# Kernel optimization log

Hardware: AMD Instinct MI355X
Metric: run time of the kernel (lower is better)

Reference implementation:

```python
import jax, jax.numpy as jnp
import numpy as np

B, S, D = 4, 2048, 1024
H = 16
HD = D // H
PF = 4096
EPS = 1e-5


def setup_inputs() -> dict:
    key = jax.random.key(0)
    ks = jax.random.split(key, 16)
    s = 1.0 / np.sqrt(D)
    inp = {
        'src': jax.random.normal(ks[0], (B, S, D), jnp.float32),
        'Wq': jax.random.normal(ks[1], (D, D), jnp.float32) * s,
        'bq': jnp.zeros((D,), jnp.float32),
        'Wk': jax.random.normal(ks[2], (D, D), jnp.float32) * s,
        'bk': jnp.zeros((D,), jnp.float32),
        'Wv': jax.random.normal(ks[3], (D, D), jnp.float32) * s,
        'bv': jnp.zeros((D,), jnp.float32),
        'Wo': jax.random.normal(ks[4], (D, D), jnp.float32) * s,
        'bo': jnp.zeros((D,), jnp.float32),
        'g1': jnp.ones((D,), jnp.float32),
        'b1': jnp.zeros((D,), jnp.float32),
        'W1': jax.random.normal(ks[5], (D, PF), jnp.float32) * s,
        'bf1': jnp.zeros((PF,), jnp.float32),
        'W2': jax.random.normal(ks[6], (PF, D), jnp.float32) * (1.0 / np.sqrt(PF)),
        'bf2': jnp.zeros((D,), jnp.float32),
        'g2': jnp.ones((D,), jnp.float32),
        'b2': jnp.zeros((D,), jnp.float32),
    }
    return inp


def _layer_norm(x, g, b):
    mu = jnp.mean(x, axis=-1, keepdims=True)
    var = jnp.mean(jnp.square(x - mu), axis=-1, keepdims=True)
    return (x - mu) * jax.lax.rsqrt(var + EPS) * g + b


def reference(src, Wq, bq, Wk, bk, Wv, bv, Wo, bo, g1, b1, W1, bf1, W2, bf2, g2, b2):
    scale = 1.0 / np.sqrt(HD)
    # QKV projections -> [B, H, S, HD]
    q = (src @ Wq + bq).reshape(B, S, H, HD).transpose(0, 2, 1, 3)
    k = (src @ Wk + bk).reshape(B, S, H, HD).transpose(0, 2, 1, 3)
    v = (src @ Wv + bv).reshape(B, S, H, HD).transpose(0, 2, 1, 3)
    # attention scores [B, H, S, S]
    attn = jax.nn.softmax(jnp.einsum('bhqd,bhkd->bhqk', q, k) * scale, axis=-1)
    x = jnp.einsum('bhqk,bhkd->bhqd', attn, v)
    x = x.transpose(0, 2, 1, 3).reshape(B, S, D)
    attn_out = x @ Wo + bo
    # residual + LN (dropout is identity at p=0)
    src1 = _layer_norm(src + attn_out, g1, b1)
    # positionwise FFN: Linear -> Dropout -> ReLU -> Linear
    ff = jax.nn.relu(src1 @ W1 + bf1) @ W2 + bf2
    return _layer_norm(src1 + ff, g2, b2)
```

## Files before the change

kernel.cpp:

```cpp
#include <hip/hip_runtime.h>

#define BB 4
#define SS 2048
#define DD 1024
#define HH 16
#define PFF 4096
#define MR 8192

typedef unsigned short u16;
typedef __attribute__((ext_vector_type(8))) short s16x8;
typedef __attribute__((ext_vector_type(4))) float f32x4v;
typedef __attribute__((ext_vector_type(16))) float f32x16;
typedef __attribute__((ext_vector_type(4))) unsigned short u16x4;
typedef __attribute__((ext_vector_type(8))) unsigned short u16x8;

__device__ inline u16 f2bf(float f) {
  union { float f; unsigned u; } v; v.f = f;
  unsigned r = v.u + 0x7FFFu + ((v.u >> 16) & 1u);
  return (u16)(r >> 16);
}

__device__ inline unsigned cvtpk_bf16(float lo, float hi) {
  unsigned r;
  asm("v_cvt_pk_bf16_f32 %0, %1, %2" : "=v"(r) : "v"(lo), "v"(hi));
  return r;
}

__device__ inline void gload16(const void* g, void* l) {
  __builtin_amdgcn_global_load_lds(
      (const __attribute__((address_space(1))) void*)g,
      (__attribute__((address_space(3))) void*)l, 16, 0, 0);
}

__device__ inline f32x4v MFMA(s16x8 a, s16x8 b, f32x4v c) {
  return __builtin_amdgcn_mfma_f32_16x16x32_bf16(a, b, c, 0, 0, 0);
}
__device__ inline f32x16 MFMA32(s16x8 a, s16x8 b, f32x16 c) {
  return __builtin_amdgcn_mfma_f32_32x32x16_bf16(a, b, c, 0, 0, 0);
}

#define RAWBAR()                          \
  do {                                    \
    asm volatile("" ::: "memory");        \
    __builtin_amdgcn_s_barrier();         \
    asm volatile("" ::: "memory");        \
  } while (0)
#define WAITVM(N) asm volatile("s_waitcnt vmcnt(" #N ")" ::: "memory")

__device__ inline s16x8 ldfrag(const u16* base, int row, int colByte) {
  return *(const s16x8*)((const char*)base + row * 128 + (colByte ^ ((row & 7) << 4)));
}

template <int BN, int RELU, int OUTBF, int SCQ>
__global__ __launch_bounds__(512, 1) void gemm256(
    const u16* __restrict__ A, const u16* __restrict__ Bt,
    const float* __restrict__ bias, float* __restrict__ Cf,
    u16* __restrict__ Cb, int M, int N, int K, int ntx) {
  constexpr int WM = (BN == 256) ? 8 : 4;
  constexpr int HM = WM / 2;
  constexpr int BUF = 8192 + BN * 32;
  __shared__ __align__(128) u16 lds[3 * BUF];
  const int t = threadIdx.x;
  const int lane = t & 63, w = t >> 6;
  const int wr = (BN == 256) ? (w >> 2) : (w >> 1);
  const int wc = (BN == 256) ? (w & 3) : (w & 1);
  const int g = lane >> 4, q = lane & 15;

  const int cpx = gridDim.x >> 3;
  const int wg = (blockIdx.x & 7) * cpx + (blockIdx.x >> 3);
  const int row0 = (wg / ntx) * 256, col0 = (wg % ntx) * BN;

  f32x4v acc[WM][4];
#pragma unroll
  for (int m = 0; m < WM; ++m)
#pragma unroll
    for (int n = 0; n < 4; ++n) acc[m][n] = (f32x4v){0.f, 0.f, 0.f, 0.f};

  const int sr0 = t >> 2, sc0 = (t & 3) * 8;
  const u16* Ag0 = A + (size_t)(row0 + sr0) * K + sc0;
  const u16* Ag1 = A + (size_t)(row0 + sr0 + 128) * K + sc0;
  const u16* Bg0 = Bt + (size_t)(col0 + sr0) * K + sc0;
  const u16* Bg1 = Bt + (size_t)(col0 + sr0 + 128) * K + sc0;
  const int wud = (t & ~63) * 8;

#define STAGE_A(kt, buf)                                          \
  do {                                                            \
    u16* ab_ = &lds[(buf) * BUF];                                 \
    gload16(Ag0 + (kt) * 32, ab_ + wud);                          \
    gload16(Ag1 + (kt) * 32, ab_ + 4096 + wud);                   \
  } while (0)
#define STAGE_B(kt, buf)                                          \
  do {                                                            \
    u16* bb_ = &lds[(buf) * BUF + 8192];                          \
    gload16(Bg0 + (kt) * 32, bb_ + wud);                          \
    if (BN == 256) gload16(Bg1 + (kt) * 32, bb_ + 4096 + wud);    \
  } while (0)

  const int NT = K / 32;
  STAGE_A(0, 0); STAGE_B(0, 0);
  STAGE_A(1, 1); STAGE_B(1, 1);
  if constexpr (BN == 256) WAITVM(4); else WAITVM(3);
  RAWBAR();

  int cur = 0, nxt = 2;
  for (int kt = 0; kt < NT; ++kt) {
    const u16* ab = &lds[cur * BUF];
    const u16* bb = ab + 8192;
    const bool pf = (kt + 2 < NT);
    if (pf) STAGE_A(kt + 2, nxt);
    s16x8 bf_[4], af_[HM];
#pragma unroll
    for (int n = 0; n < 4; ++n)
      bf_[n] = *(const s16x8*)&bb[(wc * 64 + n * 16 + q) * 32 + g * 8];
#pragma unroll
    for (int m = 0; m < HM; ++m)
      af_[m] = *(const s16x8*)&ab[(wr * (WM * 16) + m * 16 + q) * 32 + g * 8];
    RAWBAR();
    __builtin_amdgcn_s_setprio(1);
#pragma unroll
    for (int m = 0; m < HM; ++m)
#pragma unroll
      for (int n = 0; n < 4; ++n) acc[m][n] = MFMA(af_[m], bf_[n], acc[m][n]);
    __builtin_amdgcn_s_setprio(0);
    RAWBAR();
    if (pf) STAGE_B(kt + 2, nxt);
#pragma unroll
    for (int m = 0; m < HM; ++m)
      af_[m] = *(const s16x8*)&ab[(wr * (WM * 16) + (m + HM) * 16 + q) * 32 + g * 8];
    RAWBAR();
    __builtin_amdgcn_s_setprio(1);
#pragma unroll
    for (int m = 0; m < HM; ++m)
#pragma unroll
      for (int n = 0; n < 4; ++n)
        acc[m + HM][n] = MFMA(af_[m], bf_[n], acc[m + HM][n]);
    __builtin_amdgcn_s_setprio(0);
    if (kt + 1 < NT) {
      if (pf) {
        if constexpr (BN == 256) WAITVM(4); else WAITVM(3);
      } else {
        WAITVM(0);
      }
    }
    RAWBAR();
    cur = (cur == 2) ? 0 : cur + 1;
    nxt = (nxt == 2) ? 0 : nxt + 1;
  }
#undef STAGE_A
#undef STAGE_B

#pragma unroll
  for (int n = 0; n < 4; ++n) {
    const int col = col0 + wc * 64 + 16 * n + q;
    const float bv = bias[col];
#pragma unroll
    for (int m = 0; m < WM; ++m) {
#pragma unroll
      for (int r = 0; r < 4; ++r) {
        const int row = row0 + wr * (WM * 16) + 16 * m + 4 * g + r;
        float v = acc[m][n][r] + bv;
        if (RELU) v = fmaxf(v, 0.f);
        if (SCQ && col < DD) v *= 0.18033688011112042f;
        if (OUTBF) Cb[(size_t)row * N + col] = f2bf(v);
        else Cf[(size_t)row * N + col] = v;
      }
    }
  }
}

__global__ __launch_bounds__(256, 4) void attn_mfma(
    const u16* __restrict__ qkv, const u16* __restrict__ vt,
    u16* __restrict__ xb) {
  __shared__ __align__(128) u16 lds[16384];

  const int t = threadIdx.x;
  const int w = t >> 6, lane = t & 63;
  const int q = lane & 31, hi = lane >> 5;
  const int qg = w >> 1;
  const int kg = w & 1;

  const int flat = blockIdx.x;
  const int xcd = flat & 7;
  const int j = flat >> 3;
  const int bh = xcd * 8 + (j & 7);
  const int qb = j >> 3;
  const int b = bh >> 4, h = bh & 15;
  const int q0 = qb * 64;
  const int qcol = h * 64, kcol = DD + h * 64;

  const int r0 = t >> 3;
  const int sc = ((t & 7) ^ (r0 & 7)) * 8;
  const int ldst = (t & ~63) * 16;
  const u16* Ksrc = qkv + (size_t)(b * SS + r0) * 3072 + kcol + sc;
  const u16* Vsrc = vt + (size_t)(bh * 64 + r0) * SS + sc;

  {
    const u16* Qsrc = qkv + (size_t)(b * SS + q0 + r0) * 3072 + qcol + sc;
    gload16(Qsrc, (char*)lds + ldst);
    gload16(Qsrc + (size_t)32 * 3072, (char*)lds + 4096 + ldst);
  }
  WAITVM(0);
  RAWBAR();
  s16x8 qf[4];
  {
    const u16* Qw = lds + qg * 2048;
#pragma unroll
    for (int s = 0; s < 4; ++s) qf[s] = ldfrag(Qw, q, 32 * s + 16 * hi);
  }
  asm volatile("s_waitcnt lgkmcnt(0)" ::: "memory");
  __builtin_amdgcn_sched_barrier(0);
  RAWBAR();

  gload16(Ksrc, (char*)lds + ldst);
  gload16(Ksrc + (size_t)32 * 3072, (char*)lds + 4096 + ldst);
  gload16(Vsrc, (char*)lds + 8192 + ldst);
  gload16(Vsrc + 32 * SS, (char*)lds + 12288 + ldst);
  WAITVM(0);
  RAWBAR();

  s16x8 onesv;
#pragma unroll
  for (int i = 0; i < 8; ++i) onesv[i] = (short)0x3F80;

  f32x16 zf;
#pragma unroll
  for (int i = 0; i < 16; ++i) zf[i] = 0.f;

  f32x16 oac0, oac1, lacc;
#pragma unroll
  for (int i = 0; i < 16; ++i) { oac0[i] = 0.f; oac1[i] = 0.f; lacc[i] = 0.f; }

  for (int kt = 0; kt < SS / 64; ++kt) {
    const int cur = kt & 1;
    const u16* Kc = lds + cur * 8192;
    const u16* Vc = Kc + 4096;
    if (kt + 1 < SS / 64) {
      const size_t ko = (size_t)(kt + 1) * 64 * 3072;
      const int vo = (kt + 1) * 64;
      char* base = (char*)lds + (cur ^ 1) * 16384;
      gload16(Ksrc + ko, base + ldst);
      gload16(Ksrc + ko + (size_t)32 * 3072, base + 4096 + ldst);
      gload16(Vsrc + vo, base + 8192 + ldst);
      gload16(Vsrc + vo + 32 * SS, base + 12288 + ldst);
    }

    __builtin_amdgcn_s_setprio(1);
    s16x8 k0 = ldfrag(Kc, kg * 32 + q, 16 * hi);
    f32x16 sa = MFMA32(k0, qf[0], zf);
#pragma unroll
    for (int s = 1; s < 4; ++s) {
      s16x8 ks = ldfrag(Kc, kg * 32 + q, 32 * s + 16 * hi);
      sa = MFMA32(ks, qf[s], sa);
    }
    __builtin_amdgcn_s_setprio(0);

#pragma unroll
    for (int i = 0; i < 16; ++i) sa[i] = exp2f(sa[i]);

    __builtin_amdgcn_s_setprio(1);
#pragma unroll
    for (int sp = 0; sp < 2; ++sp) {
      const int rb = 8 * sp;
      unsigned x0 = cvtpk_bf16(sa[rb + 0], sa[rb + 1]);
      unsigned x1 = cvtpk_bf16(sa[rb + 2], sa[rb + 3]);
      unsigned y0 = cvtpk_bf16(sa[rb + 4], sa[rb + 5]);
      unsigned y1 = cvtpk_bf16(sa[rb + 6], sa[rb + 7]);
      asm("v_permlane32_swap_b32 %0, %1" : "+v"(x0), "+v"(y0));
      asm("v_permlane32_swap_b32 %0, %1" : "+v"(x1), "+v"(y1));
      union { unsigned u[4]; s16x8 v; } pf;
      pf.u[0] = x0; pf.u[1] = x1; pf.u[2] = y0; pf.u[3] = y1;
      s16x8 v0 = ldfrag(Vc, q, kg * 64 + 32 * sp + 16 * hi);
      s16x8 v1 = ldfrag(Vc, 32 + q, kg * 64 + 32 * sp + 16 * hi);
      oac0 = MFMA32(v0, pf.v, oac0);
      oac1 = MFMA32(v1, pf.v, oac1);
      lacc = MFMA32(onesv, pf.v, lacc);
    }
    __builtin_amdgcn_s_setprio(0);

    WAITVM(0);
    RAWBAR();
  }

  __syncthreads();
  float* red = (float*)lds;
  if (kg == 1) {
    float* myr = red + (qg * 64 + lane) * 33;
#pragma unroll
    for (int i = 0; i < 16; ++i) { myr[i] = oac0[i]; myr[16 + i] = oac1[i]; }
    myr[32] = lacc[0];
  }
  __syncthreads();
  if (kg == 0) {
    const float* pr = red + (qg * 64 + lane) * 33;
#pragma unroll
    for (int i = 0; i < 16; ++i) { oac0[i] += pr[i]; oac1[i] += pr[16 + i]; }
    const float inv = 1.f / (lacc[0] + pr[32]);
    const size_t row = (size_t)(b * SS + q0 + qg * 32 + q);
    u16* orow = xb + row * DD + qcol;
#pragma unroll
    for (int rr = 0; rr < 4; ++rr) {
      uint2 pw0, pw1;
      pw0.x = cvtpk_bf16(oac0[4 * rr] * inv, oac0[4 * rr + 1] * inv);
      pw0.y = cvtpk_bf16(oac0[4 * rr + 2] * inv, oac0[4 * rr + 3] * inv);
      pw1.x = cvtpk_bf16(oac1[4 * rr] * inv, oac1[4 * rr + 1] * inv);
      pw1.y = cvtpk_bf16(oac1[4 * rr + 2] * inv, oac1[4 * rr + 3] * inv);
      *(uint2*)(orow + 8 * rr + 4 * hi) = pw0;
      *(uint2*)(orow + 32 + 8 * rr + 4 * hi) = pw1;
    }
  }
}

__global__ __launch_bounds__(256) void cvt_bf16(const float* __restrict__ x,
                                                u16* __restrict__ y, int n4) {
  int i = blockIdx.x * 256 + threadIdx.x;
  if (i < n4) {
    float4 v = ((const float4*)x)[i];
    u16x4 o;
    o[0] = f2bf(v.x); o[1] = f2bf(v.y); o[2] = f2bf(v.z); o[3] = f2bf(v.w);
    ((u16x4*)y)[i] = o;
  }
}

__global__ __launch_bounds__(256) void transpose_w(const float* __restrict__ W,
                                                   u16* __restrict__ Wt,
                                                   int K, int N) {
  __shared__ float T[32][33];
  const int n0 = blockIdx.x * 32, k0 = blockIdx.y * 32;
  const int t = threadIdx.x;
  const int r = t >> 3, c = (t & 7) * 4;
  float4 v = *(const float4*)&W[(size_t)(k0 + r) * N + n0 + c];
  T[r][c] = v.x; T[r][c + 1] = v.y; T[r][c + 2] = v.z; T[r][c + 3] = v.w;
  __syncthreads();
  const int a = t >> 3, b0 = (t & 7) * 4;
  u16x4 o;
#pragma unroll
  for (int j = 0; j < 4; ++j) o[j] = f2bf(T[b0 + j][a]);
  *(u16x4*)&Wt[(size_t)(n0 + a) * K + k0 + b0] = o;
}

__global__ __launch_bounds__(256) void vtrans(const u16* __restrict__ qkv,
                                              u16* __restrict__ vt) {
  __shared__ u16 T[64 * 72];
  const int t = threadIdx.x;
  const int bh = blockIdx.y, b = bh >> 4, h = bh & 15;
  const int s0 = blockIdx.x * 64;
  const int vcol = 2048 + h * 64;
#pragma unroll
  for (int i = 0; i < 2; ++i) {
    int c = i * 256 + t;
    int sr = c >> 3, dc = (c & 7) * 8;
    *(u16x8*)&T[sr * 72 + dc] =
        *(const u16x8*)&qkv[(size_t)(b * SS + s0 + sr) * 3072 + vcol + dc];
  }
  __syncthreads();
#pragma unroll
  for (int i = 0; i < 2; ++i) {
    int c = i * 256 + t;
    int d = c >> 3, scnk = (c & 7) * 8;
    u16x8 o;
#pragma unroll
    for (int jj = 0; jj < 8; ++jj) o[jj] = T[(scnk + jj) * 72 + d];
    *(u16x8*)&vt[(size_t)(bh * 64 + d) * SS + s0 + scnk] = o;
  }
}

__global__ __launch_bounds__(256) void concat3(const float* __restrict__ a,
                                               const float* __restrict__ b,
                                               const float* __restrict__ c,
                                               float* __restrict__ o) {
  int i = blockIdx.x * 256 + threadIdx.x;
  if (i < 3072)
    o[i] = i < 1024 ? a[i] : (i < 2048 ? b[i - 1024] : c[i - 2048]);
}

template <int WB>
__global__ __launch_bounds__(256) void ln_res(
    const float* __restrict__ X, const float* __restrict__ R,
    const float* __restrict__ g, const float* __restrict__ b,
    float* __restrict__ Y, u16* __restrict__ Yb) {
  const int row = blockIdx.x;
  const int t = threadIdx.x;
  const size_t off = (size_t)row * DD + t * 4;

  float4 x4 = *(const float4*)&X[off];
  float4 r4 = *(const float4*)&R[off];
  float v0 = x4.x + r4.x, v1 = x4.y + r4.y, v2 = x4.z + r4.z, v3 = x4.w + r4.w;

  float s1 = v0 + v1 + v2 + v3;
  float s2 = v0 * v0 + v1 * v1 + v2 * v2 + v3 * v3;
#pragma unroll
  for (int o = 1; o < 64; o <<= 1) {
    s1 += __shfl_xor(s1, o);
    s2 += __shfl_xor(s2, o);
  }
  __shared__ float red1[4], red2[4];
  if ((t & 63) == 0) {
    red1[t >> 6] = s1;
    red2[t >> 6] = s2;
  }
  __syncthreads();
  s1 = red1[0] + red1[1] + red1[2] + red1[3];
  s2 = red2[0] + red2[1] + red2[2] + red2[3];

  const float mu = s1 * (1.f / DD);
  const float var = s2 * (1.f / DD) - mu * mu;
  const float rs = rsqrtf(var + 1e-5f);

  float4 g4 = *(const float4*)&g[t * 4];
  float4 b4 = *(const float4*)&b[t * 4];
  float4 y;
  y.x = (v0 - mu) * rs * g4.x + b4.x;
  y.y = (v1 - mu) * rs * g4.y + b4.y;
  y.z = (v2 - mu) * rs * g4.z + b4.z;
  y.w = (v3 - mu) * rs * g4.w + b4.w;
  *(float4*)&Y[off] = y;
  if (WB) {
    u16x4 o;
    o[0] = f2bf(y.x); o[1] = f2bf(y.y); o[2] = f2bf(y.z); o[3] = f2bf(y.w);
    *(u16x4*)&Yb[off] = o;
  }
}

extern "C" void kernel_launch(void* const* d_in, const int* in_sizes, int n_in,
                              void* d_out, int out_size, void* d_ws,
                              size_t ws_size, hipStream_t stream) {
  const float* src = (const float*)d_in[0];
  const float* Wq  = (const float*)d_in[1];
  const float* bq  = (const float*)d_in[2];
  const float* Wk  = (const float*)d_in[3];
  const float* bk  = (const float*)d_in[4];
  const float* Wv  = (const float*)d_in[5];
  const float* bv  = (const float*)d_in[6];
  const float* Wo  = (const float*)d_in[7];
  const float* bo  = (const float*)d_in[8];
  const float* g1  = (const float*)d_in[9];
  const float* b1  = (const float*)d_in[10];
  const float* W1  = (const float*)d_in[11];
  const float* bf1 = (const float*)d_in[12];
  const float* W2  = (const float*)d_in[13];
  const float* bf2 = (const float*)d_in[14];
  const float* g2  = (const float*)d_in[15];
  const float* b2  = (const float*)d_in[16];

  char* W = (char*)d_ws;
  u16*   wqkvT = (u16*)  (W + 0);
  u16*   woT   = (u16*)  (W + 6291456);
  u16*   w1T   = (u16*)  (W + 8388608);
  u16*   w2T   = (u16*)  (W + 16777216);
  float* bqkv  = (float*)(W + 25165824);
  u16*   srcb  = (u16*)  (W + 25178112);
  u16*   qkv   = (u16*)  (W + 41955328);
  u16*   vt    = (u16*)  (W + 92286976);
  u16*   xb    = (u16*)  (W + 109064192);
  float* pb    = (float*)(W + 125841408);
  float* s1f   = (float*)(W + 159395840);
  u16*   s1bb  = (u16*)  (W + 109064192);
  u16*   f1b   = (u16*)  (W + 41955328);
  float* f2b   = (float*)(W + 125841408);

  dim3 blk(256);

  cvt_bf16<<<8192, blk, 0, stream>>>(src, srcb, MR * DD / 4);
  transpose_w<<<dim3(32, 32), blk, 0, stream>>>(Wq, wqkvT, DD, DD);
  transpose_w<<<dim3(32, 32), blk, 0, stream>>>(Wk, wqkvT + (size_t)1024 * 1024, DD, DD);
  transpose_w<<<dim3(32, 32), blk, 0, stream>>>(Wv, wqkvT + (size_t)2048 * 1024, DD, DD);
  transpose_w<<<dim3(32, 32), blk, 0, stream>>>(Wo, woT, DD, DD);
  transpose_w<<<dim3(128, 32), blk, 0, stream>>>(W1, w1T, DD, PFF);
  transpose_w<<<dim3(32, 128), blk, 0, stream>>>(W2, w2T, PFF, DD);
  concat3<<<12, blk, 0, stream>>>(bq, bk, bv, bqkv);

  gemm256<256, 0, 1, 1><<<384, 512, 0, stream>>>(srcb, wqkvT, bqkv, nullptr,
                                                 qkv, MR, 3072, DD, 12);
  vtrans<<<dim3(32, 64), blk, 0, stream>>>(qkv, vt);
  attn_mfma<<<2048, 256, 0, stream>>>(qkv, vt, xb);
  gemm256<128, 0, 0, 0><<<256, 512, 0, stream>>>(xb, woT, bo, pb, nullptr,
                                                 MR, DD, DD, 8);
  ln_res<1><<<MR, blk, 0, stream>>>(src, pb, g1, b1, s1f, s1bb);
  gemm256<256, 1, 1, 0><<<512, 512, 0, stream>>>(s1bb, w1T, bf1, nullptr, f1b,
                                                 MR, PFF, DD, 16);
  gemm256<128, 0, 0, 0><<<256, 512, 0, stream>>>(f1b, w2T, bf2, f2b, nullptr,
                                                 MR, DD, PFF, 8);
  ln_res<0><<<MR, blk, 0, stream>>>(s1f, f2b, g2, b2, (float*)d_out, nullptr);
}
```

Measured before the change: 465.1 us.

## Triple-buffer K/V tiles in attention kernel with two-tile-deep prefetch

Moves the attention kernel's K/V staging from double to triple buffering in LDS, so loads run two tiles ahead and the end-of-iteration wait only covers the tile just consumed. This hides more global-load latency behind the MFMA work. In exchange LDS use per block rises from 32KB to 48KB and the occupancy hint drops from 4 to 3 blocks per CU, which could cut latency hiding across waves.

After: 465.6 us. About the same (+0.1%).

```diff
diff --git a/kernel.cpp b/kernel.cpp
--- a/kernel.cpp
+++ b/kernel.cpp
@@ -168,10 +168,10 @@
   }
 }
 
-__global__ __launch_bounds__(256, 4) void attn_mfma(
+__global__ __launch_bounds__(256, 3) void attn_mfma(
     const u16* __restrict__ qkv, const u16* __restrict__ vt,
     u16* __restrict__ xb) {
-  __shared__ __align__(128) u16 lds[16384];
+  __shared__ __align__(128) u16 lds[3 * 8192];
 
   const int t = threadIdx.x;
   const int w = t >> 6, lane = t & 63;
@@ -211,11 +211,20 @@
   __builtin_amdgcn_sched_barrier(0);
   RAWBAR();
 
-  gload16(Ksrc, (char*)lds + ldst);
-  gload16(Ksrc + (size_t)32 * 3072, (char*)lds + 4096 + ldst);
-  gload16(Vsrc, (char*)lds + 8192 + ldst);
-  gload16(Vsrc + 32 * SS, (char*)lds + 12288 + ldst);
-  WAITVM(0);
+#define STAGEKV(kt, bufidx)                                             \
+  do {                                                                  \
+    char* base_ = (char*)lds + (bufidx) * 16384;                        \
+    const size_t ko_ = (size_t)(kt) * 64 * 3072;                        \
+    const int vo_ = (kt) * 64;                                          \
+    gload16(Ksrc + ko_, base_ + ldst);                                  \
+    gload16(Ksrc + ko_ + (size_t)32 * 3072, base_ + 4096 + ldst);       \
+    gload16(Vsrc + vo_, base_ + 8192 + ldst);                           \
+    gload16(Vsrc + vo_ + 32 * SS, base_ + 12288 + ldst);                \
+  } while (0)
+
+  STAGEKV(0, 0);
+  STAGEKV(1, 1);
+  WAITVM(4);
   RAWBAR();
 
   s16x8 onesv;
@@ -230,19 +239,13 @@
 #pragma unroll
   for (int i = 0; i < 16; ++i) { oac0[i] = 0.f; oac1[i] = 0.f; lacc[i] = 0.f; }
 
-  for (int kt = 0; kt < SS / 64; ++kt) {
-    const int cur = kt & 1;
+  const int NT = SS / 64;
+  int cur = 0, nxt = 2;
+  for (int kt = 0; kt < NT; ++kt) {
+    const bool pf = (kt + 2 < NT);
+    if (pf) STAGEKV(kt + 2, nxt);
     const u16* Kc = lds + cur * 8192;
     const u16* Vc = Kc + 4096;
-    if (kt + 1 < SS / 64) {
-      const size_t ko = (size_t)(kt + 1) * 64 * 3072;
-      const int vo = (kt + 1) * 64;
-      char* base = (char*)lds + (cur ^ 1) * 16384;
-      gload16(Ksrc + ko, base + ldst);
-      gload16(Ksrc + ko + (size_t)32 * 3072, base + 4096 + ldst);
-      gload16(Vsrc + vo, base + 8192 + ldst);
-      gload16(Vsrc + vo + 32 * SS, base + 12288 + ldst);
-    }
 
     __builtin_amdgcn_s_setprio(1);
     s16x8 k0 = ldfrag(Kc, kg * 32 + q, 16 * hi);
@@ -267,19 +270,25 @@
       unsigned y1 = cvtpk_bf16(sa[rb + 6], sa[rb + 7]);
       asm("v_permlane32_swap_b32 %0, %1" : "+v"(x0), "+v"(y0));
       asm("v_permlane32_swap_b32 %0, %1" : "+v"(x1), "+v"(y1));
-      union { unsigned u[4]; s16x8 v; } pf;
-      pf.u[0] = x0; pf.u[1] = x1; pf.u[2] = y0; pf.u[3] = y1;
+      union { unsigned u[4]; s16x8 v; } pfv;
+      pfv.u[0] = x0; pfv.u[1] = x1; pfv.u[2] = y0; pfv.u[3] = y1;
       s16x8 v0 = ldfrag(Vc, q, kg * 64 + 32 * sp + 16 * hi);
       s16x8 v1 = ldfrag(Vc, 32 + q, kg * 64 + 32 * sp + 16 * hi);
-      oac0 = MFMA32(v0, pf.v, oac0);
-      oac1 = MFMA32(v1, pf.v, oac1);
-      lacc = MFMA32(onesv, pf.v, lacc);
+      oac0 = MFMA32(v0, pfv.v, oac0);
+      oac1 = MFMA32(v1, pfv.v, oac1);
+      lacc = MFMA32(onesv, pfv.v, lacc);
     }
     __builtin_amdgcn_s_setprio(0);
 
-    WAITVM(0);
+    if (kt + 1 < NT) {
+      if (pf) WAITVM(4);
+      else WAITVM(0);
+    }
     RAWBAR();
-  }
+    cur = (cur == 2) ? 0 : cur + 1;
+    nxt = (nxt == 2) ? 0 : nxt + 1;
+  }
+#undef STAGEKV
 
   __syncthreads();
   float* red = (float*)lds;
```

## Merge prep kernels and split-K the N=1024 GEMMs, folding partial sums into LayerNorm

Applied to the files above, without the earlier changes.

Merges the src conversion, the six weight transposes and the bias concat into one prep_all launch to cut launch overhead. When the workspace is large enough, the Wo and W2 GEMMs (N=1024, only 256 tiles) run as two sequential split-K halves writing separate fp32 partial outputs. The residual LayerNorm kernels then add the second partial. Each split GEMM has half the K loop, but the halves run back to back, so this adds launches and an extra fp32 partial write/read rather than more concurrency.

Result: slower. 480.9 us (+3.4%).

```diff
diff --git a/kernel.cpp b/kernel.cpp
--- a/kernel.cpp
+++ b/kernel.cpp
@@ -55,7 +55,7 @@
 __global__ __launch_bounds__(512, 1) void gemm256(
     const u16* __restrict__ A, const u16* __restrict__ Bt,
     const float* __restrict__ bias, float* __restrict__ Cf,
-    u16* __restrict__ Cb, int M, int N, int K, int ntx) {
+    u16* __restrict__ Cb, int M, int N, int K, int lda, int ntx) {
   constexpr int WM = (BN == 256) ? 8 : 4;
   constexpr int HM = WM / 2;
   constexpr int BUF = 8192 + BN * 32;
@@ -77,10 +77,10 @@
     for (int n = 0; n < 4; ++n) acc[m][n] = (f32x4v){0.f, 0.f, 0.f, 0.f};
 
   const int sr0 = t >> 2, sc0 = (t & 3) * 8;
-  const u16* Ag0 = A + (size_t)(row0 + sr0) * K + sc0;
-  const u16* Ag1 = A + (size_t)(row0 + sr0 + 128) * K + sc0;
-  const u16* Bg0 = Bt + (size_t)(col0 + sr0) * K + sc0;
-  const u16* Bg1 = Bt + (size_t)(col0 + sr0 + 128) * K + sc0;
+  const u16* Ag0 = A + (size_t)(row0 + sr0) * lda + sc0;
+  const u16* Ag1 = A + (size_t)(row0 + sr0 + 128) * lda + sc0;
+  const u16* Bg0 = Bt + (size_t)(col0 + sr0) * lda + sc0;
+  const u16* Bg1 = Bt + (size_t)(col0 + sr0 + 128) * lda + sc0;
   const int wud = (t & ~63) * 8;
 
 #define STAGE_A(kt, buf)                                          \
@@ -152,7 +152,7 @@
 #pragma unroll
   for (int n = 0; n < 4; ++n) {
     const int col = col0 + wc * 64 + 16 * n + q;
-    const float bv = bias[col];
+    const float bv = bias ? bias[col] : 0.f;
 #pragma unroll
     for (int m = 0; m < WM; ++m) {
 #pragma unroll
@@ -267,13 +267,13 @@
       unsigned y1 = cvtpk_bf16(sa[rb + 6], sa[rb + 7]);
       asm("v_permlane32_swap_b32 %0, %1" : "+v"(x0), "+v"(y0));
       asm("v_permlane32_swap_b32 %0, %1" : "+v"(x1), "+v"(y1));
-      union { unsigned u[4]; s16x8 v; } pf;
-      pf.u[0] = x0; pf.u[1] = x1; pf.u[2] = y0; pf.u[3] = y1;
+      union { unsigned u[4]; s16x8 v; } pfv;
+      pfv.u[0] = x0; pfv.u[1] = x1; pfv.u[2] = y0; pfv.u[3] = y1;
       s16x8 v0 = ldfrag(Vc, q, kg * 64 + 32 * sp + 16 * hi);
       s16x8 v1 = ldfrag(Vc, 32 + q, kg * 64 + 32 * sp + 16 * hi);
-      oac0 = MFMA32(v0, pf.v, oac0);
-      oac1 = MFMA32(v1, pf.v, oac1);
-      lacc = MFMA32(onesv, pf.v, lacc);
+      oac0 = MFMA32(v0, pfv.v, oac0);
+      oac1 = MFMA32(v1, pfv.v, oac1);
+      lacc = MFMA32(onesv, pfv.v, lacc);
     }
     __builtin_amdgcn_s_setprio(0);
 
@@ -310,23 +310,48 @@
   }
 }
 
-__global__ __launch_bounds__(256) void cvt_bf16(const float* __restrict__ x,
-                                                u16* __restrict__ y, int n4) {
-  int i = blockIdx.x * 256 + threadIdx.x;
-  if (i < n4) {
-    float4 v = ((const float4*)x)[i];
+__global__ __launch_bounds__(256) void prep_all(
+    const float* __restrict__ src, u16* __restrict__ srcb,
+    const float* __restrict__ Wq, const float* __restrict__ Wk,
+    const float* __restrict__ Wv, const float* __restrict__ Wo,
+    u16* __restrict__ wqkvT, u16* __restrict__ woT,
+    const float* __restrict__ W1, u16* __restrict__ w1T,
+    const float* __restrict__ W2, u16* __restrict__ w2T,
+    const float* __restrict__ bq, const float* __restrict__ bk,
+    const float* __restrict__ bvv, float* __restrict__ bqkv) {
+  const int id = blockIdx.x;
+  const int t = threadIdx.x;
+  __shared__ float T[32][33];
+
+  if (id < 8192) {
+    int i = id * 256 + t;
+    float4 v = ((const float4*)src)[i];
     u16x4 o;
     o[0] = f2bf(v.x); o[1] = f2bf(v.y); o[2] = f2bf(v.z); o[3] = f2bf(v.w);
-    ((u16x4*)y)[i] = o;
-  }
-}
-
-__global__ __launch_bounds__(256) void transpose_w(const float* __restrict__ W,
-                                                   u16* __restrict__ Wt,
-                                                   int K, int N) {
-  __shared__ float T[32][33];
-  const int n0 = blockIdx.x * 32, k0 = blockIdx.y * 32;
-  const int t = threadIdx.x;
+    ((u16x4*)srcb)[i] = o;
+    return;
+  }
+  const int id2 = id - 8192;
+  if (id2 >= 12288) {
+    int i = (id2 - 12288) * 256 + t;
+    if (i < 3072)
+      bqkv[i] = i < 1024 ? bq[i] : (i < 2048 ? bk[i - 1024] : bvv[i - 2048]);
+    return;
+  }
+  const float* W; u16* Wt; int K, N, bx, by;
+  if (id2 < 4096) {
+    const int which = id2 >> 10, tile = id2 & 1023;
+    W = (which == 0) ? Wq : (which == 1) ? Wk : (which == 2) ? Wv : Wo;
+    Wt = (which == 3) ? woT : wqkvT + (size_t)which * 1024 * 1024;
+    K = 1024; N = 1024; bx = tile & 31; by = tile >> 5;
+  } else if (id2 < 8192) {
+    const int tile = id2 - 4096;
+    W = W1; Wt = w1T; K = 1024; N = 4096; bx = tile & 127; by = tile >> 7;
+  } else {
+    const int tile = id2 - 8192;
+    W = W2; Wt = w2T; K = 4096; N = 1024; bx = tile & 31; by = tile >> 5;
+  }
+  const int n0 = bx * 32, k0 = by * 32;
   const int r = t >> 3, c = (t & 7) * 4;
   float4 v = *(const float4*)&W[(size_t)(k0 + r) * N + n0 + c];
   T[r][c] = v.x; T[r][c + 1] = v.y; T[r][c + 2] = v.z; T[r][c + 3] = v.w;
@@ -334,7 +359,7 @@
   const int a = t >> 3, b0 = (t & 7) * 4;
   u16x4 o;
 #pragma unroll
-  for (int j = 0; j < 4; ++j) o[j] = f2bf(T[b0 + j][a]);
+  for (int jj = 0; jj < 4; ++jj) o[jj] = f2bf(T[b0 + jj][a]);
   *(u16x4*)&Wt[(size_t)(n0 + a) * K + k0 + b0] = o;
 }
 
@@ -364,20 +389,12 @@
   }
 }
 
-__global__ __launch_bounds__(256) void concat3(const float* __restrict__ a,
-                                               const float* __restrict__ b,
-                                               const float* __restrict__ c,
-                                               float* __restrict__ o) {
-  int i = blockIdx.x * 256 + threadIdx.x;
-  if (i < 3072)
-    o[i] = i < 1024 ? a[i] : (i < 2048 ? b[i - 1024] : c[i - 2048]);
-}
-
-template <int WB>
+template <int WB, int ADD2>
 __global__ __launch_bounds__(256) void ln_res(
     const float* __restrict__ X, const float* __restrict__ R,
-    const float* __restrict__ g, const float* __restrict__ b,
-    float* __restrict__ Y, u16* __restrict__ Yb) {
+    const float* __restrict__ R2, const float* __restrict__ g,
+    const float* __restrict__ b, float* __restrict__ Y,
+    u16* __restrict__ Yb) {
   const int row = blockIdx.x;
   const int t = threadIdx.x;
   const size_t off = (size_t)row * DD + t * 4;
@@ -385,6 +402,10 @@
   float4 x4 = *(const float4*)&X[off];
   float4 r4 = *(const float4*)&R[off];
   float v0 = x4.x + r4.x, v1 = x4.y + r4.y, v2 = x4.z + r4.z, v3 = x4.w + r4.w;
+  if (ADD2) {
+    float4 s4 = *(const float4*)&R2[off];
+    v0 += s4.x; v1 += s4.y; v2 += s4.z; v3 += s4.w;
+  }
 
   float s1 = v0 + v1 + v2 + v3;
   float s2 = v0 * v0 + v1 * v1 + v2 * v2 + v3 * v3;
@@ -454,31 +475,50 @@
   u16*   xb    = (u16*)  (W + 109064192);
   float* pb    = (float*)(W + 125841408);
   float* s1f   = (float*)(W + 159395840);
+  float* pb2   = (float*)(W + 192950272);
   u16*   s1bb  = (u16*)  (W + 109064192);
   u16*   f1b   = (u16*)  (W + 41955328);
   float* f2b   = (float*)(W + 125841408);
-
+  float* f2b2  = pb2;
+
+  const bool sk = (ws_size >= 226504704ull);
   dim3 blk(256);
 
-  cvt_bf16<<<8192, blk, 0, stream>>>(src, srcb, MR * DD / 4);
-  transpose_w<<<dim3(32, 32), blk, 0, stream>>>(Wq, wqkvT, DD, DD);
-  transpose_w<<<dim3(32, 32), blk, 0, stream>>>(Wk, wqkvT + (size_t)1024 * 1024, DD, DD);
-  transpose_w<<<dim3(32, 32), blk, 0, stream>>>(Wv, wqkvT + (size_t)2048 * 1024, DD, DD);
-  transpose_w<<<dim3(32, 32), blk, 0, stream>>>(Wo, woT, DD, DD);
-  transpose_w<<<dim3(128, 32), blk, 0, stream>>>(W1, w1T, DD, PFF);
-  transpose_w<<<dim3(32, 128), blk, 0, stream>>>(W2, w2T, PFF, DD);
-  concat3<<<12, blk, 0, stream>>>(bq, bk, bv, bqkv);
+  prep_all<<<20492, blk, 0, stream>>>(src, srcb, Wq, Wk, Wv, Wo, wqkvT, woT,
+                                      W1, w1T, W2, w2T, bq, bk, bv, bqkv);
 
   gemm256<256, 0, 1, 1><<<384, 512, 0, stream>>>(srcb, wqkvT, bqkv, nullptr,
-                                                 qkv, MR, 3072, DD, 12);
+                                                 qkv, MR, 3072, DD, DD, 12);
   vtrans<<<dim3(32, 64), blk, 0, stream>>>(qkv, vt);
-  attn_mfma<<<2048, 256, 0, stream>>>(qkv, vt, xb);
-  gemm256<128, 0, 0, 0><<<256, 512, 0, stream>>>(xb, woT, bo, pb, nullptr,
-                                                 MR, DD, DD, 8);
-  ln_res<1><<<MR, blk, 0, stream>>>(src, pb, g1, b1, s1f, s1bb);
+  attn_mfma<<<2048, blk, 0, stream>>>(qkv, vt, xb);
+
+  if (sk) {
+    gemm256<128, 0, 0, 0><<<256, 512, 0, stream>>>(xb, woT, bo, pb, nullptr,
+                                                   MR, DD, 512, DD, 8);
+    gemm256<128, 0, 0, 0><<<256, 512, 0, stream>>>(xb + 512, woT + 512, nullptr,
+                                                   pb2, nullptr, MR, DD, 512,
+                                                   DD, 8);
+    ln_res<1, 1><<<MR, blk, 0, stream>>>(src, pb, pb2, g1, b1, s1f, s1bb);
+  } else {
+    gemm256<128, 0, 0, 0><<<256, 512, 0, stream>>>(xb, woT, bo, pb, nullptr,
+                                                   MR, DD, DD, DD, 8);
+    ln_res<1, 0><<<MR, blk, 0, stream>>>(src, pb, nullptr, g1, b1, s1f, s1bb);
+  }
+
   gemm256<256, 1, 1, 0><<<512, 512, 0, stream>>>(s1bb, w1T, bf1, nullptr, f1b,
-                                                 MR, PFF, DD, 16);
-  gemm256<128, 0, 0, 0><<<256, 512, 0, stream>>>(f1b, w2T, bf2, f2b, nullptr,
-                                                 MR, DD, PFF, 8);
-  ln_res<0><<<MR, blk, 0, stream>>>(s1f, f2b, g2, b2, (float*)d_out, nullptr);
-}
+                                                 MR, PFF, DD, DD, 16);
+  if (sk) {
+    gemm256<128, 0, 0, 0><<<256, 512, 0, stream>>>(f1b, w2T, bf2, f2b, nullptr,
+                                                   MR, DD, 2048, PFF, 8);
+    gemm256<128, 0, 0, 0><<<256, 512, 0, stream>>>(f1b + 2048, w2T + 2048,
+                                                   nullptr, f2b2, nullptr, MR,
+                                                   DD, 2048, PFF, 8);
+    ln_res<0, 1><<<MR, blk, 0, stream>>>(s1f, f2b, f2b2, g2, b2,
+                                         (float*)d_out, nullptr);
+  } else {
+    gemm256<128, 0, 0, 0><<<256, 512, 0, stream>>>(f1b, w2T, bf2, f2b, nullptr,
+                                                   MR, DD, PFF, PFF, 8);
+    ln_res<0, 0><<<MR, blk, 0, stream>>>(s1f, f2b, nullptr, g2, b2,
+                                         (float*)d_out, nullptr);
+  }
+}
```

## Fuse V transpose into QKV GEMM epilogue and drop fp32 LN1 output

Applied to the files above, without the earlier changes.

The QKV GEMM epilogue now writes the V columns straight into the transposed per-head layout used by attention, so the separate vtrans kernel and its read of the V slice go away. The first layernorm no longer writes an fp32 copy of its output, and the second layernorm reads the bf16 copy as its residual input instead. This cuts one launch and several tens of MB of global traffic. In exchange, the final residual is added at bf16 precision rather than fp32, and the V stores are 8-byte writes scattered with a large stride.

After: 453.8 us. 1.03x faster.

```diff
diff --git a/kernel.cpp b/kernel.cpp
--- a/kernel.cpp
+++ b/kernel.cpp
@@ -18,6 +18,12 @@
   union { float f; unsigned u; } v; v.f = f;
   unsigned r = v.u + 0x7FFFu + ((v.u >> 16) & 1u);
   return (u16)(r >> 16);
+}
+
+__device__ inline float bf2f(u16 x) {
+  union { unsigned u; float f; } v;
+  v.u = ((unsigned)x) << 16;
+  return v.f;
 }
 
 __device__ inline unsigned cvtpk_bf16(float lo, float hi) {
@@ -51,11 +57,12 @@
   return *(const s16x8*)((const char*)base + row * 128 + (colByte ^ ((row & 7) << 4)));
 }
 
-template <int BN, int RELU, int OUTBF, int SCQ>
+template <int BN, int RELU, int OUTBF, int SCQ, int VT>
 __global__ __launch_bounds__(512, 1) void gemm256(
     const u16* __restrict__ A, const u16* __restrict__ Bt,
     const float* __restrict__ bias, float* __restrict__ Cf,
-    u16* __restrict__ Cb, int M, int N, int K, int ntx) {
+    u16* __restrict__ Cb, u16* __restrict__ Vt, int M, int N, int K,
+    int ntx) {
   constexpr int WM = (BN == 256) ? 8 : 4;
   constexpr int HM = WM / 2;
   constexpr int BUF = 8192 + BN * 32;
@@ -152,17 +159,26 @@
 #pragma unroll
   for (int n = 0; n < 4; ++n) {
     const int col = col0 + wc * 64 + 16 * n + q;
-    const float bv = bias[col];
+    const float bv = bias ? bias[col] : 0.f;
 #pragma unroll
     for (int m = 0; m < WM; ++m) {
-#pragma unroll
-      for (int r = 0; r < 4; ++r) {
-        const int row = row0 + wr * (WM * 16) + 16 * m + 4 * g + r;
-        float v = acc[m][n][r] + bv;
-        if (RELU) v = fmaxf(v, 0.f);
-        if (SCQ && col < DD) v *= 0.18033688011112042f;
-        if (OUTBF) Cb[(size_t)row * N + col] = f2bf(v);
-        else Cf[(size_t)row * N + col] = v;
+      const int row = row0 + wr * (WM * 16) + 16 * m + 4 * g;
+      if (VT && col >= 2048) {
+        const int hd = col - 2048;
+        u16x4 o;
+#pragma unroll
+        for (int r = 0; r < 4; ++r) o[r] = f2bf(acc[m][n][r] + bv);
+        *(u16x4*)&Vt[((size_t)((row >> 11) * 16 + (hd >> 6)) * 64 +
+                      (hd & 63)) * SS + (row & 2047)] = o;
+      } else {
+#pragma unroll
+        for (int r = 0; r < 4; ++r) {
+          float v = acc[m][n][r] + bv;
+          if (RELU) v = fmaxf(v, 0.f);
+          if (SCQ && col < DD) v *= 0.18033688011112042f;
+          if (OUTBF) Cb[(size_t)(row + r) * N + col] = f2bf(v);
+          else Cf[(size_t)(row + r) * N + col] = v;
+        }
       }
     }
   }
@@ -267,13 +283,13 @@
       unsigned y1 = cvtpk_bf16(sa[rb + 6], sa[rb + 7]);
       asm("v_permlane32_swap_b32 %0, %1" : "+v"(x0), "+v"(y0));
       asm("v_permlane32_swap_b32 %0, %1" : "+v"(x1), "+v"(y1));
-      union { unsigned u[4]; s16x8 v; } pf;
-      pf.u[0] = x0; pf.u[1] = x1; pf.u[2] = y0; pf.u[3] = y1;
+      union { unsigned u[4]; s16x8 v; } pfv;
+      pfv.u[0] = x0; pfv.u[1] = x1; pfv.u[2] = y0; pfv.u[3] = y1;
       s16x8 v0 = ldfrag(Vc, q, kg * 64 + 32 * sp + 16 * hi);
       s16x8 v1 = ldfrag(Vc, 32 + q, kg * 64 + 32 * sp + 16 * hi);
-      oac0 = MFMA32(v0, pf.v, oac0);
-      oac1 = MFMA32(v1, pf.v, oac1);
-      lacc = MFMA32(onesv, pf.v, lacc);
+      oac0 = MFMA32(v0, pfv.v, oac0);
+      oac1 = MFMA32(v1, pfv.v, oac1);
+      lacc = MFMA32(onesv, pfv.v, lacc);
     }
     __builtin_amdgcn_s_setprio(0);
 
@@ -338,32 +354,6 @@
   *(u16x4*)&Wt[(size_t)(n0 + a) * K + k0 + b0] = o;
 }
 
-__global__ __launch_bounds__(256) void vtrans(const u16* __restrict__ qkv,
-                                              u16* __restrict__ vt) {
-  __shared__ u16 T[64 * 72];
-  const int t = threadIdx.x;
-  const int bh = blockIdx.y, b = bh >> 4, h = bh & 15;
-  const int s0 = blockIdx.x * 64;
-  const int vcol = 2048 + h * 64;
-#pragma unroll
-  for (int i = 0; i < 2; ++i) {
-    int c = i * 256 + t;
-    int sr = c >> 3, dc = (c & 7) * 8;
-    *(u16x8*)&T[sr * 72 + dc] =
-        *(const u16x8*)&qkv[(size_t)(b * SS + s0 + sr) * 3072 + vcol + dc];
-  }
-  __syncthreads();
-#pragma unroll
-  for (int i = 0; i < 2; ++i) {
-    int c = i * 256 + t;
-    int d = c >> 3, scnk = (c & 7) * 8;
-    u16x8 o;
-#pragma unroll
-    for (int jj = 0; jj < 8; ++jj) o[jj] = T[(scnk + jj) * 72 + d];
-    *(u16x8*)&vt[(size_t)(bh * 64 + d) * SS + s0 + scnk] = o;
-  }
-}
-
 __global__ __launch_bounds__(256) void concat3(const float* __restrict__ a,
                                                const float* __restrict__ b,
                                                const float* __restrict__ c,
@@ -373,18 +363,26 @@
     o[i] = i < 1024 ? a[i] : (i < 2048 ? b[i - 1024] : c[i - 2048]);
 }
 
-template <int WB>
+template <int WB, int WF, int XBF>
 __global__ __launch_bounds__(256) void ln_res(
-    const float* __restrict__ X, const float* __restrict__ R,
-    const float* __restrict__ g, const float* __restrict__ b,
-    float* __restrict__ Y, u16* __restrict__ Yb) {
+    const float* __restrict__ Xf, const u16* __restrict__ Xb,
+    const float* __restrict__ R, const float* __restrict__ g,
+    const float* __restrict__ b, float* __restrict__ Y,
+    u16* __restrict__ Yb) {
   const int row = blockIdx.x;
   const int t = threadIdx.x;
   const size_t off = (size_t)row * DD + t * 4;
 
-  float4 x4 = *(const float4*)&X[off];
+  float v0, v1, v2, v3;
+  if (XBF) {
+    u16x4 x4 = *(const u16x4*)&Xb[off];
+    v0 = bf2f(x4[0]); v1 = bf2f(x4[1]); v2 = bf2f(x4[2]); v3 = bf2f(x4[3]);
+  } else {
+    float4 x4 = *(const float4*)&Xf[off];
+    v0 = x4.x; v1 = x4.y; v2 = x4.z; v3 = x4.w;
+  }
   float4 r4 = *(const float4*)&R[off];
-  float v0 = x4.x + r4.x, v1 = x4.y + r4.y, v2 = x4.z + r4.z, v3 = x4.w + r4.w;
+  v0 += r4.x; v1 += r4.y; v2 += r4.z; v3 += r4.w;
 
   float s1 = v0 + v1 + v2 + v3;
   float s2 = v0 * v0 + v1 * v1 + v2 * v2 + v3 * v3;
@@ -413,7 +411,7 @@
   y.y = (v1 - mu) * rs * g4.y + b4.y;
   y.z = (v2 - mu) * rs * g4.z + b4.z;
   y.w = (v3 - mu) * rs * g4.w + b4.w;
-  *(float4*)&Y[off] = y;
+  if (WF) *(float4*)&Y[off] = y;
   if (WB) {
     u16x4 o;
     o[0] = f2bf(y.x); o[1] = f2bf(y.y); o[2] = f2bf(y.z); o[3] = f2bf(y.w);
@@ -453,7 +451,6 @@
   u16*   vt    = (u16*)  (W + 92286976);
   u16*   xb    = (u16*)  (W + 109064192);
   float* pb    = (float*)(W + 125841408);
-  float* s1f   = (float*)(W + 159395840);
   u16*   s1bb  = (u16*)  (W + 109064192);
   u16*   f1b   = (u16*)  (W + 41955328);
   float* f2b   = (float*)(W + 125841408);
@@ -469,16 +466,17 @@
   transpose_w<<<dim3(32, 128), blk, 0, stream>>>(W2, w2T, PFF, DD);
   concat3<<<12, blk, 0, stream>>>(bq, bk, bv, bqkv);
 
-  gemm256<256, 0, 1, 1><<<384, 512, 0, stream>>>(srcb, wqkvT, bqkv, nullptr,
-                                                 qkv, MR, 3072, DD, 12);
-  vtrans<<<dim3(32, 64), blk, 0, stream>>>(qkv, vt);
-  attn_mfma<<<2048, 256, 0, stream>>>(qkv, vt, xb);
-  gemm256<128, 0, 0, 0><<<256, 512, 0, stream>>>(xb, woT, bo, pb, nullptr,
-                                                 MR, DD, DD, 8);
-  ln_res<1><<<MR, blk, 0, stream>>>(src, pb, g1, b1, s1f, s1bb);
-  gemm256<256, 1, 1, 0><<<512, 512, 0, stream>>>(s1bb, w1T, bf1, nullptr, f1b,
-                                                 MR, PFF, DD, 16);
-  gemm256<128, 0, 0, 0><<<256, 512, 0, stream>>>(f1b, w2T, bf2, f2b, nullptr,
-                                                 MR, DD, PFF, 8);
-  ln_res<0><<<MR, blk, 0, stream>>>(s1f, f2b, g2, b2, (float*)d_out, nullptr);
-}
+  gemm256<256, 0, 1, 1, 1><<<384, 512, 0, stream>>>(
+      srcb, wqkvT, bqkv, nullptr, qkv, vt, MR, 3072, DD, 12);
+  attn_mfma<<<2048, blk, 0, stream>>>(qkv, vt, xb);
+  gemm256<128, 0, 0, 0, 0><<<256, 512, 0, stream>>>(
+      xb, woT, bo, pb, nullptr, nullptr, MR, DD, DD, 8);
+  ln_res<1, 0, 0><<<MR, blk, 0, stream>>>(src, nullptr, pb, g1, b1, nullptr,
+                                          s1bb);
+  gemm256<256, 1, 1, 0, 0><<<512, 512, 0, stream>>>(
+      s1bb, w1T, bf1, nullptr, f1b, nullptr, MR, PFF, DD, 16);
+  gemm256<128, 0, 0, 0, 0><<<256, 512, 0, stream>>>(
+      f1b, w2T, bf2, f2b, nullptr, nullptr, MR, DD, PFF, 8);
+  ln_res<0, 1, 1><<<MR, blk, 0, stream>>>(nullptr, s1bb, f2b, g2, b2,
+                                          (float*)d_out, nullptr);
+}
```
